# Kernel tuning notes

Measured on AMD Instinct MI355X. Metric: run time of the kernel, lower is better.

Reference implementation:

```python
import jax, jax.numpy as jnp
import numpy as np

WEIGHT = 0.1  # init kwarg `weight`


def setup_inputs() -> dict:
    key = jax.random.key(0)
    k1, k2, k3 = jax.random.split(key, 3)
    B, H, W, M = 32, 640, 640, 256
    seg_preds = jax.random.normal(k1, (B, 1, H, W), dtype=jnp.float32)
    bboxes = jax.random.uniform(k2, (M, 4), dtype=jnp.float32)  # normalized xywh in [0,1)
    batch_idx = jax.random.randint(k3, (M,), 0, B, dtype=jnp.int32)
    is_seg = jnp.zeros((B,), dtype=bool)  # all detection images
    return {"seg_preds": seg_preds, "bboxes": bboxes, "batch_idx": batch_idx, "is_seg": is_seg}


def _boxes_to_masks(bboxes, batch_idx, B, H, W):
    # Vectorized rasterization of all M boxes at once (no per-box loop).
    cx = bboxes[:, 0] * W
    cy = bboxes[:, 1] * H
    bw = bboxes[:, 2] * W
    bh = bboxes[:, 3] * H
    # clamp to [0, dim-1] then truncate to int (values are non-negative, so
    # astype(int) == torch .long() truncation)
    x1 = jnp.clip(cx - bw / 2.0, 0, W - 1).astype(jnp.int32)
    y1 = jnp.clip(cy - bh / 2.0, 0, H - 1).astype(jnp.int32)
    x2 = jnp.clip(cx + bw / 2.0, 0, W - 1).astype(jnp.int32)
    y2 = jnp.clip(cy + bh / 2.0, 0, H - 1).astype(jnp.int32)
    ys = jnp.arange(H, dtype=jnp.int32)
    xs = jnp.arange(W, dtype=jnp.int32)
    in_y = (ys[None, :] >= y1[:, None]) & (ys[None, :] <= y2[:, None])  # [M,H]
    in_x = (xs[None, :] >= x1[:, None]) & (xs[None, :] <= x2[:, None])  # [M,W]
    box_mask = (in_y[:, :, None] & in_x[:, None, :]).astype(jnp.float32)  # [M,H,W]
    # union of boxes per image = clip(sum, 0, 1)
    per_img = jax.ops.segment_sum(box_mask, batch_idx, num_segments=B)  # [B,H,W]
    return jnp.clip(per_img, 0.0, 1.0)[:, None, :, :]  # [B,1,H,W]


def reference(seg_preds, bboxes, batch_idx, is_seg):
    B, _, H, W = seg_preds.shape
    pseudo = _boxes_to_masks(bboxes, batch_idx, B, H, W)
    det_mask = (~is_seg).astype(jnp.float32)  # [B]
    pseudo = pseudo * det_mask[:, None, None, None]
    # BCEWithLogitsLoss(reduction='mean'), numerically stable form
    x = seg_preds
    y = pseudo
    bce = jnp.mean(jnp.maximum(x, 0.0) - x * y + jnp.log1p(jnp.exp(-jnp.abs(x))))
    has_det = (jnp.sum(det_mask) > 0).astype(x.dtype)
    return WEIGHT * bce * has_det
```

## Files before the change

### kernel.cpp

```cpp
#include <hip/hip_runtime.h>
#include <hip/hip_bf16.h>

constexpr int B  = 32;
constexpr int H  = 640;
constexpr int Wd = 640;
constexpr int M  = 256;

constexpr int CHUNKS       = 100;
constexpr int F4_PER_IMG   = H * Wd / 4;
constexpr int F4_PER_BLOCK = F4_PER_IMG / CHUNKS;
constexpr int NBLK         = B * CHUNKS;

constexpr unsigned long long COUNT_UNIT = 1ull << 52;
constexpr unsigned long long VAL_MASK   = COUNT_UNIT - 1ull;
constexpr unsigned long long POISON64   = 0xAAAAAAAAAAAAAAAAull;
constexpr unsigned long long POISON_HI  = POISON64 >> 52;

constexpr size_t WS_IMGACC_OFF = 4096;

__global__ __launch_bounds__(256) void fused_bce(
    const float* __restrict__ seg_preds,
    const float* __restrict__ bboxes,
    const int* __restrict__ batch_idx,
    const unsigned char* __restrict__ is_seg,
    unsigned long long* __restrict__ gacc,
    unsigned long long* __restrict__ imgacc,
    float* __restrict__ out)
{
    const int img   = blockIdx.x / CHUNKS;
    const int chunk = blockIdx.x % CHUNKS;

    __shared__ ushort4 sbox[M];
    __shared__ int scount;
    __shared__ float wsum[4];

    const int p_start = chunk * F4_PER_BLOCK * 4;
    const int row_lo  = p_start / Wd;
    const int row_hi  = (p_start + F4_PER_BLOCK * 4 - 1) / Wd;

    if (threadIdx.x == 0) scount = 0;
    __syncthreads();

    if (threadIdx.x < M) {
        const float4 bb = ((const float4*)bboxes)[threadIdx.x];
        if (batch_idx[threadIdx.x] == img) {
            float cx = bb.x * 640.0f, cy = bb.y * 640.0f;
            float bw = bb.z * 640.0f, bh = bb.w * 640.0f;
            float x1f = fminf(fmaxf(cx - bw * 0.5f, 0.0f), 639.0f);
            float y1f = fminf(fmaxf(cy - bh * 0.5f, 0.0f), 639.0f);
            float x2f = fminf(fmaxf(cx + bw * 0.5f, 0.0f), 639.0f);
            float y2f = fminf(fmaxf(cy + bh * 0.5f, 0.0f), 639.0f);
            int y1 = (int)y1f, y2 = (int)y2f;
            if (y1 <= row_hi && y2 >= row_lo) {
                ushort4 bx;
                bx.x = (unsigned short)(int)x1f;
                bx.y = (unsigned short)y1;
                bx.z = (unsigned short)(int)x2f;
                bx.w = (unsigned short)y2;
                int slot = atomicAdd(&scount, 1);
                sbox[slot] = bx;
            }
        }
    }
    __syncthreads();
    const int  ncnt = scount;
    const bool det  = (is_seg[img] == 0);

    const float4* __restrict__ xin =
        (const float4*)(seg_preds + (size_t)img * H * Wd);

    float acc = 0.0f;
    #pragma unroll
    for (int k = 0; k < 4; ++k) {
        const int    f4 = chunk * F4_PER_BLOCK + k * 256 + threadIdx.x;
        const float4 v  = xin[f4];
        const int p   = f4 * 4;
        const int row = p / Wd;
        const int col = p - row * Wd;

        unsigned covm = 0u;
        if (det) {
            for (int i = 0; i < ncnt; ++i) {
                ushort4 bx = sbox[i];
                if (row >= (int)bx.y && row <= (int)bx.w) {
                    int lo = max((int)bx.x - col, 0);
                    int hi = min((int)bx.z - col, 3);
                    if (lo <= hi) covm |= ((1u << (hi - lo + 1)) - 1u) << lo;
                    if (covm == 0xFu) break;
                }
            }
        }
        const float vals[4] = {v.x, v.y, v.z, v.w};
        #pragma unroll
        for (int j = 0; j < 4; ++j) {
            float xv = vals[j];
            float a  = fabsf(xv);
            float sp = __logf(1.0f + __expf(-a));
            float term = fmaxf(xv, 0.0f) + sp;
            if (covm & (1u << j)) term -= xv;
            acc += term;
        }
    }

    for (int off = 32; off > 0; off >>= 1)
        acc += __shfl_down(acc, off, 64);
    const int lane = threadIdx.x & 63;
    const int wid  = threadIdx.x >> 6;
    if (lane == 0) wsum[wid] = acc;
    __syncthreads();

    if (threadIdx.x == 0) {
        float p = wsum[0] + wsum[1] + wsum[2] + wsum[3];
        unsigned long long my =
            (unsigned long long)((double)p * 1048576.0 + 0.5) + COUNT_UNIT;
        unsigned long long old = atomicAdd(&imgacc[img * 32], my);
        unsigned long long cnt = old >> 52;
        if (cnt == (unsigned long long)(CHUNKS - 1) ||
            cnt == POISON_HI + (unsigned long long)(CHUNKS - 1)) {
            unsigned long long base =
                (cnt == (unsigned long long)(CHUNKS - 1)) ? 0ull : POISON64;
            unsigned long long img_total =
                ((old - base) & VAL_MASK) + (my & VAL_MASK);
            atomicExch(&imgacc[img * 32], 0ull);
            unsigned long long g_old = atomicAdd(gacc, img_total + COUNT_UNIT);
            unsigned long long gc = g_old >> 52;
            if (gc == (unsigned long long)(B - 1) ||
                gc == POISON_HI + (unsigned long long)(B - 1)) {
                unsigned long long gbase =
                    (gc == (unsigned long long)(B - 1)) ? 0ull : POISON64;
                unsigned long long total =
                    ((g_old - gbase) & VAL_MASK) + img_total;
                atomicExch(gacc, 0ull);
                int nd = 0;
                for (int b = 0; b < B; ++b) nd += (is_seg[b] == 0) ? 1 : 0;
                double hd   = (nd > 0) ? 1.0 : 0.0;
                double mean = ((double)total * (1.0 / 1048576.0))
                              / (double)((size_t)B * H * Wd);
                out[0] = (float)(0.1 * mean * hd);
            }
        }
    }
}

extern "C" void kernel_launch(void* const* d_in, const int* in_sizes, int n_in,
                              void* d_out, int out_size, void* d_ws, size_t ws_size,
                              hipStream_t stream)
{
    const float*         seg_preds = (const float*)d_in[0];
    const float*         bboxes    = (const float*)d_in[1];
    const int*           batch_idx = (const int*)d_in[2];
    const unsigned char* is_seg    = (const unsigned char*)d_in[3];

    unsigned long long* gacc   = (unsigned long long*)d_ws;
    unsigned long long* imgacc = (unsigned long long*)((char*)d_ws + WS_IMGACC_OFF);
    float*              out    = (float*)d_out;

    fused_bce<<<NBLK, 256, 0, stream>>>(seg_preds, bboxes, batch_idx, is_seg,
                                        gacc, imgacc, out);
}
```

Measured before the change: 25.24 us.

## Precompute per-block row coverage bitmask in shared memory instead of per-pixel box scan

Each block first builds a shared-memory bitmask over its covered rows: one 32-bit word per 32 columns, with each word computed by scanning the relevant boxes once. Pixel processing then replaces the per-thread loop over all boxes with a single shared lookup and a bit extract. The loss terms are also split into two accumulators, one for softplus+relu and one for the covered x values. This removes divergent per-pixel box loops at the cost of one more barrier and a small bitmask build phase.

```diff
diff --git a/kernel.cpp b/kernel.cpp
--- a/kernel.cpp
+++ b/kernel.cpp
@@ -10,6 +10,9 @@
 constexpr int F4_PER_IMG   = H * Wd / 4;
 constexpr int F4_PER_BLOCK = F4_PER_IMG / CHUNKS;
 constexpr int NBLK         = B * CHUNKS;
+
+constexpr int NROWS_MAX = 8;
+constexpr int WPR       = 20;
 
 constexpr unsigned long long COUNT_UNIT = 1ull << 52;
 constexpr unsigned long long VAL_MASK   = COUNT_UNIT - 1ull;
@@ -32,16 +35,20 @@
 
     __shared__ ushort4 sbox[M];
     __shared__ int scount;
+    __shared__ unsigned sbm[NROWS_MAX * WPR];
     __shared__ float wsum[4];
 
     const int p_start = chunk * F4_PER_BLOCK * 4;
     const int row_lo  = p_start / Wd;
     const int row_hi  = (p_start + F4_PER_BLOCK * 4 - 1) / Wd;
+    const int nrows   = row_hi - row_lo + 1;
+
+    const bool det = (is_seg[img] == 0);
 
     if (threadIdx.x == 0) scount = 0;
     __syncthreads();
 
-    if (threadIdx.x < M) {
+    if (threadIdx.x < M && det) {
         const float4 bb = ((const float4*)bboxes)[threadIdx.x];
         if (batch_idx[threadIdx.x] == img) {
             float cx = bb.x * 640.0f, cy = bb.y * 640.0f;
@@ -63,44 +70,51 @@
         }
     }
     __syncthreads();
-    const int  ncnt = scount;
-    const bool det  = (is_seg[img] == 0);
+    const int ncnt = scount;
+
+    for (int i = threadIdx.x; i < nrows * WPR; i += 256) {
+        const int r    = row_lo + i / WPR;
+        const int w32  = (i % WPR) << 5;
+        unsigned m = 0u;
+        for (int bi = 0; bi < ncnt; ++bi) {
+            ushort4 bx = sbox[bi];
+            if (r >= (int)bx.y && r <= (int)bx.w) {
+                int lo = max((int)bx.x - w32, 0);
+                int hi = min((int)bx.z - w32, 31);
+                if (lo <= hi)
+                    m |= (0xFFFFFFFFu >> (31 - hi)) & (0xFFFFFFFFu << lo);
+            }
+        }
+        sbm[i] = m;
+    }
+    __syncthreads();
 
     const float4* __restrict__ xin =
         (const float4*)(seg_preds + (size_t)img * H * Wd);
 
-    float acc = 0.0f;
+    float accA = 0.0f;
+    float accB = 0.0f;
     #pragma unroll
     for (int k = 0; k < 4; ++k) {
         const int    f4 = chunk * F4_PER_BLOCK + k * 256 + threadIdx.x;
         const float4 v  = xin[f4];
-        const int p   = f4 * 4;
-        const int row = p / Wd;
-        const int col = p - row * Wd;
+        const int p    = f4 * 4;
+        const int row  = p / Wd;
+        const int col  = p - row * Wd;
+        const unsigned word = sbm[(row - row_lo) * WPR + (col >> 5)];
+        const unsigned cov4 = (word >> (col & 31)) & 0xFu;
 
-        unsigned covm = 0u;
-        if (det) {
-            for (int i = 0; i < ncnt; ++i) {
-                ushort4 bx = sbox[i];
-                if (row >= (int)bx.y && row <= (int)bx.w) {
-                    int lo = max((int)bx.x - col, 0);
-                    int hi = min((int)bx.z - col, 3);
-                    if (lo <= hi) covm |= ((1u << (hi - lo + 1)) - 1u) << lo;
-                    if (covm == 0xFu) break;
-                }
-            }
-        }
         const float vals[4] = {v.x, v.y, v.z, v.w};
         #pragma unroll
         for (int j = 0; j < 4; ++j) {
             float xv = vals[j];
             float a  = fabsf(xv);
             float sp = __logf(1.0f + __expf(-a));
-            float term = fmaxf(xv, 0.0f) + sp;
-            if (covm & (1u << j)) term -= xv;
-            acc += term;
+            accA += fmaxf(xv, 0.0f) + sp;
+            accB += (cov4 & (1u << j)) ? xv : 0.0f;
         }
     }
+    float acc = accA - accB;
 
     for (int off = 32; off > 0; off >>= 1)
         acc += __shfl_down(acc, off, 64);
```

New measurement: 20.61 us, median of 2. -18.3%, faster.
